# Performance work log

Hardware: AMD Instinct MI355X
Metric: run time of the kernel (lower is better)

Reference implementation:

```python
import jax, jax.numpy as jnp
import numpy as np

B, R, D, H, C = 256, 100, 6168, 128, 100  # batch, replicas, in_dim, hidden, classes


def setup_inputs() -> dict:
    key = jax.random.key(0)
    k1, k2, k3, k4, k5, k6 = jax.random.split(key, 6)
    # binary input features (texas dataset is binary; original casts to bool)
    x = jax.random.randint(k1, (B, D), 0, 2).astype(jnp.int32)
    # Bernoulli(0.5) flip mask, one per replica per feature
    noise = jax.random.randint(k2, (B, R, D), 0, 2).astype(jnp.int32)
    s1 = 1.0 / np.sqrt(D)
    W1 = jax.random.uniform(k3, (D, H), minval=-s1, maxval=s1, dtype=jnp.float32)
    b1 = jax.random.uniform(k4, (H,), minval=-s1, maxval=s1, dtype=jnp.float32)
    s2 = 1.0 / np.sqrt(H)
    W2 = jax.random.uniform(k5, (H, C), minval=-s2, maxval=s2, dtype=jnp.float32)
    b2 = jax.random.uniform(k6, (C,), minval=-s2, maxval=s2, dtype=jnp.float32)
    return {"x": x, "noise": noise, "W1": W1, "b1": b1, "W2": W2, "b2": b2}


def reference(x, noise, W1, b1, W2, b2):
    # np.invert(x, where=noise) on booleans == flip bit where noise==1
    xb = x[:, None, :]                                   # [B,1,D]
    x_noisy = jnp.where(noise == 1, 1 - xb, xb).astype(W1.dtype)  # [B,R,D]
    h = jnp.tanh(jnp.einsum('brd,dh->brh', x_noisy, W1) + b1)      # [B,R,H]
    logits = jnp.einsum('brh,hc->brc', h, W2) + b2                 # [B,R,C]
    return logits.mean(axis=1)                                     # [B,C]
```

## Files before the change

### kernel.cpp

```cpp
#include <hip/hip_runtime.h>
#include <hip/hip_bf16.h>

#define NB 256
#define NR 100
#define ND 6168
#define DP 6176
#define NH 128
#define NC 100
#define CP 112
#define KSTEP 32
#define NSTEP (DP / KSTEP)

typedef __attribute__((ext_vector_type(8))) __bf16 bf16x8;
typedef __attribute__((ext_vector_type(4))) float f32x4;
typedef __attribute__((ext_vector_type(4))) int i32x4;
typedef __attribute__((ext_vector_type(4))) unsigned int u32x4;

#define BAR() do { asm volatile("s_waitcnt lgkmcnt(0)" ::: "memory"); \
                   __builtin_amdgcn_s_barrier(); } while (0)

__global__ void prep_w1t(const float* __restrict__ W1, __hip_bfloat16* __restrict__ W1T) {
  __shared__ float tile[KSTEP][NH + 1];
  const int d0 = blockIdx.x * KSTEP;
  const int t = threadIdx.x;
#pragma unroll
  for (int p = 0; p < (KSTEP * NH) / 256; ++p) {
    int idx = p * 256 + t;
    int dd = idx >> 7;
    int h  = idx & 127;
    int d  = d0 + dd;
    tile[dd][h] = (d < ND) ? W1[d * NH + h] : 0.f;
  }
  __syncthreads();
#pragma unroll
  for (int p = 0; p < (KSTEP * NH) / 256; ++p) {
    int idx = p * 256 + t;
    int h  = idx >> 5;
    int dd = idx & 31;
    W1T[h * DP + d0 + dd] = __float2bfloat16(tile[dd][h]);
  }
}

__global__ void prep_w2t(const float* __restrict__ W2, __hip_bfloat16* __restrict__ W2T) {
  int t = blockIdx.x * 256 + threadIdx.x;
  if (t < CP * NH) {
    int c = t >> 7;
    int h = t & 127;
    float v = (c < NC) ? W2[h * NC + c] : 0.f;
    W2T[t] = __float2bfloat16(v);
  }
}

__launch_bounds__(256, 1)
__global__ void fused_main(const int* __restrict__ x,
                           const int* __restrict__ noise,
                           const __hip_bfloat16* __restrict__ W1T,
                           const float* __restrict__ b1,
                           const __hip_bfloat16* __restrict__ W2T,
                           const float* __restrict__ b2,
                           float* __restrict__ out) {
  __shared__ __align__(16) char lds[53312];
  unsigned int* xpair = (unsigned int*)lds;
  char* const BF0 = lds + 12352;
  char* const BF1 = BF0 + 20480;

  const int tid  = threadIdx.x;
  const int lane = tid & 63;
  const int w    = tid >> 6;
  const int lq   = lane >> 4;
  const int lm   = lane & 15;
  const int b    = blockIdx.x;

  const int r  = tid >> 1;
  const int kh = tid & 1;
  const bool rvalid = (r < NR);

  const int*  nbase = noise + (long)b * NR * ND + (long)r * ND + kh * 16;
  const char* bsrc  = (const char*)W1T + (long)r * DP * 2 + kh * 32;

  f32x4 acc[8][2] = {};

  auto ISSUE = [&](int s, i32x4* ra, i32x4* rb) {
    i32x4 z = {0, 0, 0, 0};
    const long o = (long)s * KSTEP;
#pragma unroll
    for (int j = 0; j < 4; ++j) {
      int k0 = s * KSTEP + kh * 16 + j * 4;
      ra[j] = (rvalid && k0 + 4 <= ND) ? *(const i32x4*)(nbase + o + j * 4) : z;
    }
    rb[0] = *(const i32x4*)(bsrc + o * 2);
    rb[1] = *(const i32x4*)(bsrc + o * 2 + 16);
  };

  auto STORE = [&](int s, const i32x4* ra, const i32x4* rb, char* buf) {
    u32x4 xp0 = *(const u32x4*)(xpair + s * 16 + kh * 8);
    u32x4 xp1 = *(const u32x4*)(xpair + s * 16 + kh * 8 + 4);
    unsigned pk[8];
#pragma unroll
    for (int p = 0; p < 8; ++p) {
      unsigned n0 = (unsigned)ra[p >> 1][(p & 1) * 2];
      unsigned n1 = (unsigned)ra[p >> 1][(p & 1) * 2 + 1];
      unsigned xv = (p < 4) ? xp0[p] : xp1[p - 4];
      pk[p] = ((n0 | (n1 << 16)) ^ xv) * 0x3F80u;
    }
    u32x4 t0 = {pk[0], pk[1], pk[2], pk[3]};
    u32x4 t1 = {pk[4], pk[5], pk[6], pk[7]};
    *(u32x4*)(buf + r * 80 + kh * 32)          = t0;
    *(u32x4*)(buf + r * 80 + kh * 32 + 16)     = t1;
    *(i32x4*)(buf + 10240 + r * 80 + kh * 32)      = rb[0];
    *(i32x4*)(buf + 10240 + r * 80 + kh * 32 + 16) = rb[1];
  };

  auto COMPUTE = [&](const char* buf) {
    const char* Bb = buf + 10240;
    bf16x8 bf0 = *(const bf16x8*)(Bb + (w * 32 + lm) * 80 + lq * 16);
    bf16x8 bf1 = *(const bf16x8*)(Bb + (w * 32 + 16 + lm) * 80 + lq * 16);
#pragma unroll
    for (int mf = 0; mf < 8; ++mf) {
      bf16x8 af = *(const bf16x8*)(buf + (mf * 16 + lm) * 80 + lq * 16);
      acc[mf][0] = __builtin_amdgcn_mfma_f32_16x16x32_bf16(af, bf0, acc[mf][0], 0, 0, 0);
      acc[mf][1] = __builtin_amdgcn_mfma_f32_16x16x32_bf16(af, bf1, acc[mf][1], 0, 0, 0);
    }
  };

  i32x4 raA[4], rbA[2], raB[4], rbB[2];

  ISSUE(0, raA, rbA);
  ISSUE(1, raB, rbB);
  {
    const int* xb = x + b * ND;
    for (int i = tid; i < DP / 2; i += 256) {
      unsigned p = 0;
      if (2 * i + 1 < ND) {
        int2 v = *(const int2*)(xb + 2 * i);
        p = ((unsigned)v.x & 1u) | (((unsigned)v.y & 1u) << 16);
      }
      xpair[i] = p;
    }
  }
  BAR();
  STORE(0, raA, rbA, BF0);
  ISSUE(2, raA, rbA);
  BAR();

  for (int s = 0; s < NSTEP; s += 2) {
    COMPUTE(BF0);
    if (s + 1 < NSTEP) STORE(s + 1, raB, rbB, BF1);
    if (s + 3 < NSTEP) ISSUE(s + 3, raB, rbB);
    BAR();
    if (s + 1 < NSTEP) {
      COMPUTE(BF1);
      if (s + 2 < NSTEP) STORE(s + 2, raA, rbA, BF0);
      if (s + 4 < NSTEP) ISSUE(s + 4, raA, rbA);
      BAR();
    }
  }

  __hip_bfloat16* h_tile = (__hip_bfloat16*)lds;
  float* partial = (float*)(lds + 34816);

#pragma unroll
  for (int nf = 0; nf < 2; ++nf) {
    int hcol = w * 32 + nf * 16 + lm;
    float bb = b1[hcol];
#pragma unroll
    for (int mf = 0; mf < 8; ++mf) {
#pragma unroll
      for (int rg = 0; rg < 4; ++rg) {
        int m = mf * 16 + lq * 4 + rg;
        h_tile[m * 136 + hcol] = __float2bfloat16(tanhf(acc[mf][nf][rg] + bb));
      }
    }
  }
  __syncthreads();

  f32x4 acc2[2][7] = {};
#pragma unroll
  for (int ks = 0; ks < 4; ++ks) {
    bf16x8 a2_0 = *(const bf16x8*)((const unsigned short*)h_tile + (w * 32 + lm) * 136 + ks * 32 + lq * 8);
    bf16x8 a2_1 = *(const bf16x8*)((const unsigned short*)h_tile + (w * 32 + 16 + lm) * 136 + ks * 32 + lq * 8);
#pragma unroll
    for (int nf = 0; nf < 7; ++nf) {
      bf16x8 b2f = *(const bf16x8*)((const unsigned short*)W2T + (nf * 16 + lm) * NH + ks * 32 + lq * 8);
      acc2[0][nf] = __builtin_amdgcn_mfma_f32_16x16x32_bf16(a2_0, b2f, acc2[0][nf], 0, 0, 0);
      acc2[1][nf] = __builtin_amdgcn_mfma_f32_16x16x32_bf16(a2_1, b2f, acc2[1][nf], 0, 0, 0);
    }
  }

#pragma unroll
  for (int mf2 = 0; mf2 < 2; ++mf2) {
    int mbase = w * 32 + mf2 * 16 + lq * 4;
#pragma unroll
    for (int nf = 0; nf < 7; ++nf) {
      float ssum = 0.f;
#pragma unroll
      for (int rg = 0; rg < 4; ++rg) {
        int m = mbase + rg;
        ssum += (m < NR) ? acc2[mf2][nf][rg] : 0.f;
      }
      ssum += __shfl_xor(ssum, 16, 64);
      ssum += __shfl_xor(ssum, 32, 64);
      if (lq == 0) partial[(w * 2 + mf2) * 112 + nf * 16 + lm] = ssum;
    }
  }
  __syncthreads();

  if (tid < NC) {
    float fsum = 0.f;
#pragma unroll
    for (int p = 0; p < 8; ++p) fsum += partial[p * 112 + tid];
    out[b * NC + tid] = fsum * (1.f / NR) + b2[tid];
  }
}

extern "C" void kernel_launch(void* const* d_in, const int* in_sizes, int n_in,
                              void* d_out, int out_size, void* d_ws, size_t ws_size,
                              hipStream_t stream) {
  (void)in_sizes; (void)n_in; (void)out_size; (void)ws_size;
  const int* x     = (const int*)d_in[0];
  const int* noise = (const int*)d_in[1];
  const float* W1  = (const float*)d_in[2];
  const float* b1  = (const float*)d_in[3];
  const float* W2  = (const float*)d_in[4];
  const float* b2  = (const float*)d_in[5];
  float* out = (float*)d_out;

  __hip_bfloat16* W1T = (__hip_bfloat16*)d_ws;
  __hip_bfloat16* W2T = (__hip_bfloat16*)((char*)d_ws + (size_t)NH * DP * 2);

  prep_w1t<<<DP / KSTEP, 256, 0, stream>>>(W1, W1T);
  prep_w2t<<<(CP * NH + 255) / 256, 256, 0, stream>>>(W2, W2T);
  fused_main<<<NB, 256, 0, stream>>>(x, noise, W1T, b1, W2T, b2, out);
}
```

Before: 224.8 us.

## Load noise and W1T in 128-wide K groups with deeper register prefetch

The main loop now fetches 128 K-columns per thread (16 noise vectors plus 8 W1T vectors) two groups ahead, instead of one 32-wide step at a time. Each thread pair splits the staging work, with one thread writing the noise-derived A tile and the other the W1T B tile. The padded K dimension grows to 6272 so the groups divide evenly. sched_barrier guards are added around the barrier. The aim is longer, more coalesced global loads with more bytes in flight to hide memory latency, at the cost of much higher register use (48 i32x4 buffers) and some extra padding work.

New measurement: 376.8 us. 1.68x slower.

```diff
diff --git a/kernel.cpp b/kernel.cpp
--- a/kernel.cpp
+++ b/kernel.cpp
@@ -4,20 +4,26 @@
 #define NB 256
 #define NR 100
 #define ND 6168
-#define DP 6176
+#define DP 6272
 #define NH 128
 #define NC 100
 #define CP 112
 #define KSTEP 32
-#define NSTEP (DP / KSTEP)
+#define NG (DP / 128)
+#define NT (DP / KSTEP)
 
 typedef __attribute__((ext_vector_type(8))) __bf16 bf16x8;
 typedef __attribute__((ext_vector_type(4))) float f32x4;
 typedef __attribute__((ext_vector_type(4))) int i32x4;
 typedef __attribute__((ext_vector_type(4))) unsigned int u32x4;
 
-#define BAR() do { asm volatile("s_waitcnt lgkmcnt(0)" ::: "memory"); \
-                   __builtin_amdgcn_s_barrier(); } while (0)
+#define BAR() do { \
+  __builtin_amdgcn_sched_barrier(0); \
+  asm volatile("s_waitcnt lgkmcnt(0)"); \
+  __builtin_amdgcn_sched_barrier(0); \
+  __builtin_amdgcn_s_barrier(); \
+  __builtin_amdgcn_sched_barrier(0); \
+} while (0)
 
 __global__ void prep_w1t(const float* __restrict__ W1, __hip_bfloat16* __restrict__ W1T) {
   __shared__ float tile[KSTEP][NH + 1];
@@ -59,9 +65,9 @@
                            const __hip_bfloat16* __restrict__ W2T,
                            const float* __restrict__ b2,
                            float* __restrict__ out) {
-  __shared__ __align__(16) char lds[53312];
+  __shared__ __align__(16) char lds[53504];
   unsigned int* xpair = (unsigned int*)lds;
-  char* const BF0 = lds + 12352;
+  char* const BF0 = lds + 12544;
   char* const BF1 = BF0 + 20480;
 
   const int tid  = threadIdx.x;
@@ -75,40 +81,51 @@
   const int kh = tid & 1;
   const bool rvalid = (r < NR);
 
-  const int*  nbase = noise + (long)b * NR * ND + (long)r * ND + kh * 16;
-  const char* bsrc  = (const char*)W1T + (long)r * DP * 2 + kh * 32;
+  const int*  nrow  = noise + (long)b * NR * ND + (long)r * ND;
+  const char* wrow  = (const char*)W1T + (long)r * DP * 2 + (kh ^ 1) * 128;
 
   f32x4 acc[8][2] = {};
-
-  auto ISSUE = [&](int s, i32x4* ra, i32x4* rb) {
+  i32x4 nA[16], nB[16], wA[8], wB[8];
+
+  auto ISSUE_N = [&](int g, i32x4* n) {
     i32x4 z = {0, 0, 0, 0};
-    const long o = (long)s * KSTEP;
-#pragma unroll
-    for (int j = 0; j < 4; ++j) {
-      int k0 = s * KSTEP + kh * 16 + j * 4;
-      ra[j] = (rvalid && k0 + 4 <= ND) ? *(const i32x4*)(nbase + o + j * 4) : z;
-    }
-    rb[0] = *(const i32x4*)(bsrc + o * 2);
-    rb[1] = *(const i32x4*)(bsrc + o * 2 + 16);
-  };
-
-  auto STORE = [&](int s, const i32x4* ra, const i32x4* rb, char* buf) {
-    u32x4 xp0 = *(const u32x4*)(xpair + s * 16 + kh * 8);
-    u32x4 xp1 = *(const u32x4*)(xpair + s * 16 + kh * 8 + 4);
-    unsigned pk[8];
-#pragma unroll
-    for (int p = 0; p < 8; ++p) {
-      unsigned n0 = (unsigned)ra[p >> 1][(p & 1) * 2];
-      unsigned n1 = (unsigned)ra[p >> 1][(p & 1) * 2 + 1];
-      unsigned xv = (p < 4) ? xp0[p] : xp1[p - 4];
-      pk[p] = ((n0 | (n1 << 16)) ^ xv) * 0x3F80u;
-    }
-    u32x4 t0 = {pk[0], pk[1], pk[2], pk[3]};
-    u32x4 t1 = {pk[4], pk[5], pk[6], pk[7]};
-    *(u32x4*)(buf + r * 80 + kh * 32)          = t0;
-    *(u32x4*)(buf + r * 80 + kh * 32 + 16)     = t1;
-    *(i32x4*)(buf + 10240 + r * 80 + kh * 32)      = rb[0];
-    *(i32x4*)(buf + 10240 + r * 80 + kh * 32 + 16) = rb[1];
+    const int base = g * 128 + kh * 64;
+#pragma unroll
+    for (int j = 0; j < 16; ++j) {
+      int k0 = base + j * 4;
+      n[j] = (rvalid && k0 + 4 <= ND) ? *(const i32x4*)(nrow + base + j * 4) : z;
+    }
+  };
+  auto ISSUE_W = [&](int g, i32x4* wv) {
+    const char* src = wrow + g * 256;
+#pragma unroll
+    for (int j = 0; j < 8; ++j) wv[j] = *(const i32x4*)(src + j * 16);
+  };
+
+  auto STORE_T = [&](const i32x4* n, const i32x4* wv, int g, int p, char* buf) {
+    if (kh == (p >> 1)) {
+      const int rb = (p & 1) * 8;
+      u32x4 xp[4];
+#pragma unroll
+      for (int c = 0; c < 4; ++c) xp[c] = *(const u32x4*)(xpair + g * 64 + p * 16 + c * 4);
+      unsigned pk[16];
+#pragma unroll
+      for (int q = 0; q < 16; ++q) {
+        unsigned n0 = (unsigned)n[rb + (q >> 1)][(q & 1) * 2];
+        unsigned n1 = (unsigned)n[rb + (q >> 1)][(q & 1) * 2 + 1];
+        pk[q] = ((n0 | (n1 << 16)) ^ xp[q >> 2][q & 3]) * 0x3F80u;
+      }
+#pragma unroll
+      for (int c = 0; c < 4; ++c) {
+        u32x4 t = {pk[c * 4], pk[c * 4 + 1], pk[c * 4 + 2], pk[c * 4 + 3]};
+        *(u32x4*)(buf + r * 80 + c * 16) = t;
+      }
+    } else {
+      const int rb = (p & 1) * 4;
+#pragma unroll
+      for (int c = 0; c < 4; ++c)
+        *(i32x4*)(buf + 10240 + r * 80 + c * 16) = wv[rb + c];
+    }
   };
 
   auto COMPUTE = [&](const char* buf) {
@@ -123,10 +140,8 @@
     }
   };
 
-  i32x4 raA[4], rbA[2], raB[4], rbB[2];
-
-  ISSUE(0, raA, rbA);
-  ISSUE(1, raB, rbB);
+  ISSUE_N(0, nA); ISSUE_W(0, wA);
+  ISSUE_N(1, nB); ISSUE_W(1, wB);
   {
     const int* xb = x + b * ND;
     for (int i = tid; i < DP / 2; i += 256) {
@@ -139,23 +154,33 @@
     }
   }
   BAR();
-  STORE(0, raA, rbA, BF0);
-  ISSUE(2, raA, rbA);
+  STORE_T(nA, wA, 0, 0, BF0);
   BAR();
 
-  for (int s = 0; s < NSTEP; s += 2) {
-    COMPUTE(BF0);
-    if (s + 1 < NSTEP) STORE(s + 1, raB, rbB, BF1);
-    if (s + 3 < NSTEP) ISSUE(s + 3, raB, rbB);
-    BAR();
-    if (s + 1 < NSTEP) {
-      COMPUTE(BF1);
-      if (s + 2 < NSTEP) STORE(s + 2, raA, rbA, BF0);
-      if (s + 4 < NSTEP) ISSUE(s + 4, raA, rbA);
-      BAR();
-    }
-  }
-
+#define GROUP_BODY(g, curN, curW, nxtN, nxtW)                         \
+  do {                                                                \
+    COMPUTE(BF0);                                      \
+    STORE_T(curN, curW, (g), 1, BF1);                  \
+    BAR();                                                            \
+    COMPUTE(BF1);                                      \
+    STORE_T(curN, curW, (g), 2, BF0);                  \
+    BAR();                                                            \
+    COMPUTE(BF0);                                      \
+    STORE_T(curN, curW, (g), 3, BF1);                  \
+    if ((g) + 2 < NG) { ISSUE_N((g) + 2, curN); ISSUE_W((g) + 2, curW); } \
+    BAR();                                                            \
+    COMPUTE(BF1);                                      \
+    if (4 * (g) + 4 < NT) STORE_T(nxtN, nxtW, (g) + 1, 0, BF0);       \
+    BAR();                                                            \
+  } while (0)
+
+  for (int gg = 0; gg < NG; gg += 2) {
+    GROUP_BODY(gg, nA, wA, nB, wB);
+    if (gg + 1 < NG) GROUP_BODY(gg + 1, nB, wB, nA, wA);
+  }
+#undef GROUP_BODY
+
+  __syncthreads();
   __hip_bfloat16* h_tile = (__hip_bfloat16*)lds;
   float* partial = (float*)(lds + 34816);
 
```

## Split replicas across two blocks and move the replica mean before W2

Applied to the files above, without the earlier changes.

Each batch row is now handled by two blocks, each covering 50 replicas, which doubles the grid to 512 blocks and allows two blocks per CU through smaller LDS and launch bounds. Because the mean is linear, the tanh outputs are averaged over replicas before the second layer. The second GEMM then becomes a small fp32 matrix-vector product in a new combine kernel, so the W2 transpose prep kernel is dropped. This is meant to spread the noise-streaming work over more CUs and remove the second MFMA stage, at the cost of an extra kernel launch and a round trip through global memory for the partial sums.

Result: slower. 232.6 us (+3.5%).

```diff
diff --git a/kernel.cpp b/kernel.cpp
--- a/kernel.cpp
+++ b/kernel.cpp
@@ -3,13 +3,15 @@
 
 #define NB 256
 #define NR 100
+#define NRH 50
 #define ND 6168
 #define DP 6176
 #define NH 128
 #define NC 100
-#define CP 112
 #define KSTEP 32
 #define NSTEP (DP / KSTEP)
+#define MT 64
+#define W1T_BYTES ((size_t)NH * DP * 2)
 
 typedef __attribute__((ext_vector_type(8))) __bf16 bf16x8;
 typedef __attribute__((ext_vector_type(4))) float f32x4;
@@ -41,89 +43,75 @@
   }
 }
 
-__global__ void prep_w2t(const float* __restrict__ W2, __hip_bfloat16* __restrict__ W2T) {
-  int t = blockIdx.x * 256 + threadIdx.x;
-  if (t < CP * NH) {
-    int c = t >> 7;
-    int h = t & 127;
-    float v = (c < NC) ? W2[h * NC + c] : 0.f;
-    W2T[t] = __float2bfloat16(v);
-  }
-}
-
-__launch_bounds__(256, 1)
+__launch_bounds__(256, 2)
 __global__ void fused_main(const int* __restrict__ x,
                            const int* __restrict__ noise,
                            const __hip_bfloat16* __restrict__ W1T,
                            const float* __restrict__ b1,
-                           const __hip_bfloat16* __restrict__ W2T,
-                           const float* __restrict__ b2,
-                           float* __restrict__ out) {
-  __shared__ __align__(16) char lds[53312];
+                           float* __restrict__ partials) {
+  __shared__ __align__(16) char lds[43072];
   unsigned int* xpair = (unsigned int*)lds;
   char* const BF0 = lds + 12352;
-  char* const BF1 = BF0 + 20480;
+  char* const BF1 = BF0 + 15360;
 
   const int tid  = threadIdx.x;
   const int lane = tid & 63;
   const int w    = tid >> 6;
   const int lq   = lane >> 4;
   const int lm   = lane & 15;
-  const int b    = blockIdx.x;
-
-  const int r  = tid >> 1;
-  const int kh = tid & 1;
-  const bool rvalid = (r < NR);
-
-  const int*  nbase = noise + (long)b * NR * ND + (long)r * ND + kh * 16;
-  const char* bsrc  = (const char*)W1T + (long)r * DP * 2 + kh * 32;
-
-  f32x4 acc[8][2] = {};
+  const int bid  = blockIdx.x;
+  const int b    = bid >> 1;
+  const int half = bid & 1;
+
+  const int ar = tid >> 2;
+  const int kc = tid & 3;
+  const int grow = half * NRH + ((ar < NRH) ? ar : (NRH - 1));
+  const int* nrow = noise + (size_t)b * NR * ND + (size_t)grow * ND;
+
+  const int br = tid >> 1;
+  const int bh = tid & 1;
+  const char* bsrc = (const char*)W1T + (size_t)br * DP * 2 + bh * 32;
+
+  f32x4 acc[4][2] = {};
 
   auto ISSUE = [&](int s, i32x4* ra, i32x4* rb) {
     i32x4 z = {0, 0, 0, 0};
-    const long o = (long)s * KSTEP;
-#pragma unroll
-    for (int j = 0; j < 4; ++j) {
-      int k0 = s * KSTEP + kh * 16 + j * 4;
-      ra[j] = (rvalid && k0 + 4 <= ND) ? *(const i32x4*)(nbase + o + j * 4) : z;
-    }
-    rb[0] = *(const i32x4*)(bsrc + o * 2);
-    rb[1] = *(const i32x4*)(bsrc + o * 2 + 16);
+    const int k0 = s * KSTEP + kc * 8;
+    ra[0] = (k0 + 4 <= ND) ? *(const i32x4*)(nrow + k0)     : z;
+    ra[1] = (k0 + 8 <= ND) ? *(const i32x4*)(nrow + k0 + 4) : z;
+    const long o = (long)s * 64;
+    rb[0] = *(const i32x4*)(bsrc + o);
+    rb[1] = *(const i32x4*)(bsrc + o + 16);
   };
 
   auto STORE = [&](int s, const i32x4* ra, const i32x4* rb, char* buf) {
-    u32x4 xp0 = *(const u32x4*)(xpair + s * 16 + kh * 8);
-    u32x4 xp1 = *(const u32x4*)(xpair + s * 16 + kh * 8 + 4);
-    unsigned pk[8];
-#pragma unroll
-    for (int p = 0; p < 8; ++p) {
+    u32x4 xp = *(const u32x4*)(xpair + s * 16 + kc * 4);
+    unsigned pk[4];
+#pragma unroll
+    for (int p = 0; p < 4; ++p) {
       unsigned n0 = (unsigned)ra[p >> 1][(p & 1) * 2];
       unsigned n1 = (unsigned)ra[p >> 1][(p & 1) * 2 + 1];
-      unsigned xv = (p < 4) ? xp0[p] : xp1[p - 4];
-      pk[p] = ((n0 | (n1 << 16)) ^ xv) * 0x3F80u;
-    }
-    u32x4 t0 = {pk[0], pk[1], pk[2], pk[3]};
-    u32x4 t1 = {pk[4], pk[5], pk[6], pk[7]};
-    *(u32x4*)(buf + r * 80 + kh * 32)          = t0;
-    *(u32x4*)(buf + r * 80 + kh * 32 + 16)     = t1;
-    *(i32x4*)(buf + 10240 + r * 80 + kh * 32)      = rb[0];
-    *(i32x4*)(buf + 10240 + r * 80 + kh * 32 + 16) = rb[1];
+      pk[p] = ((n0 | (n1 << 16)) ^ xp[p]) * 0x3F80u;
+    }
+    u32x4 t = {pk[0], pk[1], pk[2], pk[3]};
+    *(u32x4*)(buf + ar * 80 + kc * 16) = t;
+    *(i32x4*)(buf + 5120 + br * 80 + bh * 32)      = rb[0];
+    *(i32x4*)(buf + 5120 + br * 80 + bh * 32 + 16) = rb[1];
   };
 
   auto COMPUTE = [&](const char* buf) {
-    const char* Bb = buf + 10240;
+    const char* Bb = buf + 5120;
     bf16x8 bf0 = *(const bf16x8*)(Bb + (w * 32 + lm) * 80 + lq * 16);
     bf16x8 bf1 = *(const bf16x8*)(Bb + (w * 32 + 16 + lm) * 80 + lq * 16);
 #pragma unroll
-    for (int mf = 0; mf < 8; ++mf) {
+    for (int mf = 0; mf < 4; ++mf) {
       bf16x8 af = *(const bf16x8*)(buf + (mf * 16 + lm) * 80 + lq * 16);
       acc[mf][0] = __builtin_amdgcn_mfma_f32_16x16x32_bf16(af, bf0, acc[mf][0], 0, 0, 0);
       acc[mf][1] = __builtin_amdgcn_mfma_f32_16x16x32_bf16(af, bf1, acc[mf][1], 0, 0, 0);
     }
   };
 
-  i32x4 raA[4], rbA[2], raB[4], rbB[2];
+  i32x4 raA[2], rbA[2], raB[2], rbB[2];
 
   ISSUE(0, raA, rbA);
   ISSUE(1, raB, rbB);
@@ -156,60 +144,41 @@
     }
   }
 
-  __hip_bfloat16* h_tile = (__hip_bfloat16*)lds;
-  float* partial = (float*)(lds + 34816);
-
 #pragma unroll
   for (int nf = 0; nf < 2; ++nf) {
     int hcol = w * 32 + nf * 16 + lm;
     float bb = b1[hcol];
-#pragma unroll
-    for (int mf = 0; mf < 8; ++mf) {
+    float ssum = 0.f;
+#pragma unroll
+    for (int mf = 0; mf < 4; ++mf) {
 #pragma unroll
       for (int rg = 0; rg < 4; ++rg) {
         int m = mf * 16 + lq * 4 + rg;
-        h_tile[m * 136 + hcol] = __float2bfloat16(tanhf(acc[mf][nf][rg] + bb));
+        float tv = tanhf(acc[mf][nf][rg] + bb);
+        ssum += (m < NRH) ? tv : 0.f;
       }
     }
-  }
+    ssum += __shfl_xor(ssum, 16, 64);
+    ssum += __shfl_xor(ssum, 32, 64);
+    if (lq == 0) partials[(size_t)bid * NH + hcol] = ssum;
+  }
+}
+
+__global__ void combine(const float* __restrict__ partials,
+                        const float* __restrict__ W2,
+                        const float* __restrict__ b2,
+                        float* __restrict__ out) {
+  __shared__ float hbar[NH];
+  const int b = blockIdx.x;
+  const int t = threadIdx.x;
+  if (t < NH)
+    hbar[t] = (partials[(size_t)(2 * b) * NH + t] + partials[(size_t)(2 * b + 1) * NH + t]) * (1.0f / NR);
   __syncthreads();
-
-  f32x4 acc2[2][7] = {};
-#pragma unroll
-  for (int ks = 0; ks < 4; ++ks) {
-    bf16x8 a2_0 = *(const bf16x8*)((const unsigned short*)h_tile + (w * 32 + lm) * 136 + ks * 32 + lq * 8);
-    bf16x8 a2_1 = *(const bf16x8*)((const unsigned short*)h_tile + (w * 32 + 16 + lm) * 136 + ks * 32 + lq * 8);
-#pragma unroll
-    for (int nf = 0; nf < 7; ++nf) {
-      bf16x8 b2f = *(const bf16x8*)((const unsigned short*)W2T + (nf * 16 + lm) * NH + ks * 32 + lq * 8);
-      acc2[0][nf] = __builtin_amdgcn_mfma_f32_16x16x32_bf16(a2_0, b2f, acc2[0][nf], 0, 0, 0);
-      acc2[1][nf] = __builtin_amdgcn_mfma_f32_16x16x32_bf16(a2_1, b2f, acc2[1][nf], 0, 0, 0);
-    }
-  }
-
-#pragma unroll
-  for (int mf2 = 0; mf2 < 2; ++mf2) {
-    int mbase = w * 32 + mf2 * 16 + lq * 4;
-#pragma unroll
-    for (int nf = 0; nf < 7; ++nf) {
-      float ssum = 0.f;
-#pragma unroll
-      for (int rg = 0; rg < 4; ++rg) {
-        int m = mbase + rg;
-        ssum += (m < NR) ? acc2[mf2][nf][rg] : 0.f;
-      }
-      ssum += __shfl_xor(ssum, 16, 64);
-      ssum += __shfl_xor(ssum, 32, 64);
-      if (lq == 0) partial[(w * 2 + mf2) * 112 + nf * 16 + lm] = ssum;
-    }
-  }
-  __syncthreads();
-
-  if (tid < NC) {
-    float fsum = 0.f;
-#pragma unroll
-    for (int p = 0; p < 8; ++p) fsum += partial[p * 112 + tid];
-    out[b * NC + tid] = fsum * (1.f / NR) + b2[tid];
+  if (t < NC) {
+    float s = b2[t];
+#pragma unroll 8
+    for (int h = 0; h < NH; ++h) s += hbar[h] * W2[h * NC + t];
+    out[b * NC + t] = s;
   }
 }
 
@@ -226,9 +195,9 @@
   float* out = (float*)d_out;
 
   __hip_bfloat16* W1T = (__hip_bfloat16*)d_ws;
-  __hip_bfloat16* W2T = (__hip_bfloat16*)((char*)d_ws + (size_t)NH * DP * 2);
+  float* partials = (float*)((char*)d_ws + W1T_BYTES);
 
   prep_w1t<<<DP / KSTEP, 256, 0, stream>>>(W1, W1T);
-  prep_w2t<<<(CP * NH + 255) / 256, 256, 0, stream>>>(W2, W2T);
-  fused_main<<<NB, 256, 0, stream>>>(x, noise, W1T, b1, W2T, b2, out);
-}
+  fused_main<<<2 * NB, 256, 0, stream>>>(x, noise, W1T, b1, partials);
+  combine<<<NB, 128, 0, stream>>>(partials, W2, b2, out);
+}
```
